# Kernel tuning notes

Hardware: AMD Instinct MI355X
Metric: run time of the kernel (lower is better)

The kernel has to match this reference:

```python
import jax, jax.numpy as jnp
import numpy as np

B, S, D = 64, 2048, 512

def setup_inputs() -> dict:
    key = jax.random.key(0)
    k1, k2 = jax.random.split(key)
    features = jax.random.normal(k1, (B, S, D), dtype=jnp.float32)
    # lengths in [1, S] so every sample has at least one valid timestep
    lengths = jax.random.randint(k2, (B,), 1, S + 1, dtype=jnp.int64)
    return {"features": features, "lengths": lengths}

def reference(features, lengths):
    # mask[b, s] = s < lengths[b]
    mask = (jnp.arange(features.shape[1])[None, :] < lengths[:, None])  # [B, S]
    masked_sum = jnp.einsum('bsd,bs->bd', features, mask.astype(features.dtype))
    pooled = masked_sum / lengths.astype(features.dtype)[:, None]  # [B, D]
    return pooled
```

## Files before the change

kernel.cpp:

```cpp
#include <hip/hip_runtime.h>


#define DDIM 512
#define TPB  128
#define NSPLIT_MAX 32

__device__ __forceinline__ void acc4(float4& a, const float4& v) {
    a.x += v.x; a.y += v.y; a.z += v.z; a.w += v.w;
}

__global__ void __launch_bounds__(TPB)
pool_partial(const float* __restrict__ feat, const int* __restrict__ lengths,
             float* __restrict__ ws, int S, int nsplit, int chunk) {
    const int b     = blockIdx.x;
    const int split = blockIdx.y;
    const int tid   = threadIdx.x;
    const int len   = lengths[b];

    const int s0 = split * chunk;
    const int s1 = min(s0 + chunk, len);

    float4 a0 = {0.f, 0.f, 0.f, 0.f};
    float4 a1 = {0.f, 0.f, 0.f, 0.f};
    float4 a2 = {0.f, 0.f, 0.f, 0.f};
    float4 a3 = {0.f, 0.f, 0.f, 0.f};

    const float4* __restrict__ base =
        reinterpret_cast<const float4*>(feat + (size_t)b * S * DDIM) + tid;
    const int ld4 = DDIM / 4;

    int s = s0;
    for (; s + 3 < s1; s += 4) {
        float4 v0 = base[(size_t)(s + 0) * ld4];
        float4 v1 = base[(size_t)(s + 1) * ld4];
        float4 v2 = base[(size_t)(s + 2) * ld4];
        float4 v3 = base[(size_t)(s + 3) * ld4];
        acc4(a0, v0); acc4(a1, v1); acc4(a2, v2); acc4(a3, v3);
    }
    for (; s < s1; ++s) {
        float4 v = base[(size_t)s * ld4];
        acc4(a0, v);
    }
    acc4(a0, a1); acc4(a2, a3); acc4(a0, a2);

    float4* wsp = reinterpret_cast<float4*>(ws + ((size_t)b * nsplit + split) * DDIM) + tid;
    *wsp = a0;
}

__global__ void __launch_bounds__(TPB)
pool_final(const float* __restrict__ ws, const int* __restrict__ lengths,
           float* __restrict__ out, int nsplit) {
    const int b   = blockIdx.x;
    const int tid = threadIdx.x;
    float4 acc = {0.f, 0.f, 0.f, 0.f};
    const float4* wsp = reinterpret_cast<const float4*>(ws + (size_t)b * nsplit * DDIM) + tid;
    for (int p = 0; p < nsplit; ++p) {
        acc4(acc, wsp[(size_t)p * (DDIM / 4)]);
    }
    const float inv = 1.0f / (float)lengths[b];
    float4 r = {acc.x * inv, acc.y * inv, acc.z * inv, acc.w * inv};
    reinterpret_cast<float4*>(out + (size_t)b * DDIM)[tid] = r;
}

__global__ void __launch_bounds__(TPB)
pool_direct(const float* __restrict__ feat, const int* __restrict__ lengths,
            float* __restrict__ out, int S) {
    const int b   = blockIdx.x;
    const int tid = threadIdx.x;
    const int len = lengths[b];
    float4 a0 = {0.f, 0.f, 0.f, 0.f};
    float4 a1 = {0.f, 0.f, 0.f, 0.f};
    float4 a2 = {0.f, 0.f, 0.f, 0.f};
    float4 a3 = {0.f, 0.f, 0.f, 0.f};
    const float4* __restrict__ base =
        reinterpret_cast<const float4*>(feat + (size_t)b * S * DDIM) + tid;
    const int ld4 = DDIM / 4;
    int s = 0;
    for (; s + 3 < len; s += 4) {
        float4 v0 = base[(size_t)(s + 0) * ld4];
        float4 v1 = base[(size_t)(s + 1) * ld4];
        float4 v2 = base[(size_t)(s + 2) * ld4];
        float4 v3 = base[(size_t)(s + 3) * ld4];
        acc4(a0, v0); acc4(a1, v1); acc4(a2, v2); acc4(a3, v3);
    }
    for (; s < len; ++s) { float4 v = base[(size_t)s * ld4]; acc4(a0, v); }
    acc4(a0, a1); acc4(a2, a3); acc4(a0, a2);
    const float inv = 1.0f / (float)len;
    float4 r = {a0.x * inv, a0.y * inv, a0.z * inv, a0.w * inv};
    reinterpret_cast<float4*>(out + (size_t)b * DDIM)[tid] = r;
}

extern "C" void kernel_launch(void* const* d_in, const int* in_sizes, int n_in,
                              void* d_out, int out_size, void* d_ws, size_t ws_size,
                              hipStream_t stream) {
    const float* feat    = (const float*)d_in[0];
    const int*   lengths = (const int*)d_in[1];
    float*       out     = (float*)d_out;

    const int B = in_sizes[1];
    const int S = in_sizes[0] / (B * DDIM);

    const size_t per_split = (size_t)B * DDIM * sizeof(float);
    int nsplit = (int)(ws_size / per_split);
    if (nsplit > NSPLIT_MAX) nsplit = NSPLIT_MAX;

    if (nsplit >= 2) {
        const int chunk = (S + nsplit - 1) / nsplit;
        float* ws = (float*)d_ws;
        dim3 grid1(B, nsplit);
        pool_partial<<<grid1, TPB, 0, stream>>>(feat, lengths, ws, S, nsplit, chunk);
        pool_final<<<B, TPB, 0, stream>>>(ws, lengths, out, nsplit);
    } else {
        pool_direct<<<B, TPB, 0, stream>>>(feat, lengths, out, S);
    }
}
```

Measured before the change: 36.12 us.

## Replace two-pass split reduction with length-balanced atomic accumulation

```diff
diff --git a/kernel.cpp b/kernel.cpp
--- a/kernel.cpp
+++ b/kernel.cpp
@@ -3,21 +3,23 @@
 
 #define DDIM 512
 #define TPB  128
-#define NSPLIT_MAX 32
+#define NSPLIT 32
 
 __device__ __forceinline__ void acc4(float4& a, const float4& v) {
     a.x += v.x; a.y += v.y; a.z += v.z; a.w += v.w;
 }
 
 __global__ void __launch_bounds__(TPB)
-pool_partial(const float* __restrict__ feat, const int* __restrict__ lengths,
-             float* __restrict__ ws, int S, int nsplit, int chunk) {
+pool_atomic(const float* __restrict__ feat, const int* __restrict__ lengths,
+            float* __restrict__ out, int S) {
     const int b     = blockIdx.x;
     const int split = blockIdx.y;
     const int tid   = threadIdx.x;
     const int len   = lengths[b];
 
+    const int chunk = (len + NSPLIT - 1) / NSPLIT;
     const int s0 = split * chunk;
+    if (s0 >= len) return;
     const int s1 = min(s0 + chunk, len);
 
     float4 a0 = {0.f, 0.f, 0.f, 0.f};
@@ -30,12 +32,17 @@
     const int ld4 = DDIM / 4;
 
     int s = s0;
-    for (; s + 3 < s1; s += 4) {
+    for (; s + 7 < s1; s += 8) {
         float4 v0 = base[(size_t)(s + 0) * ld4];
         float4 v1 = base[(size_t)(s + 1) * ld4];
         float4 v2 = base[(size_t)(s + 2) * ld4];
         float4 v3 = base[(size_t)(s + 3) * ld4];
+        float4 v4 = base[(size_t)(s + 4) * ld4];
+        float4 v5 = base[(size_t)(s + 5) * ld4];
+        float4 v6 = base[(size_t)(s + 6) * ld4];
+        float4 v7 = base[(size_t)(s + 7) * ld4];
         acc4(a0, v0); acc4(a1, v1); acc4(a2, v2); acc4(a3, v3);
+        acc4(a0, v4); acc4(a1, v5); acc4(a2, v6); acc4(a3, v7);
     }
     for (; s < s1; ++s) {
         float4 v = base[(size_t)s * ld4];
@@ -43,23 +50,12 @@
     }
     acc4(a0, a1); acc4(a2, a3); acc4(a0, a2);
 
-    float4* wsp = reinterpret_cast<float4*>(ws + ((size_t)b * nsplit + split) * DDIM) + tid;
-    *wsp = a0;
-}
-
-__global__ void __launch_bounds__(TPB)
-pool_final(const float* __restrict__ ws, const int* __restrict__ lengths,
-           float* __restrict__ out, int nsplit) {
-    const int b   = blockIdx.x;
-    const int tid = threadIdx.x;
-    float4 acc = {0.f, 0.f, 0.f, 0.f};
-    const float4* wsp = reinterpret_cast<const float4*>(ws + (size_t)b * nsplit * DDIM) + tid;
-    for (int p = 0; p < nsplit; ++p) {
-        acc4(acc, wsp[(size_t)p * (DDIM / 4)]);
-    }
-    const float inv = 1.0f / (float)lengths[b];
-    float4 r = {acc.x * inv, acc.y * inv, acc.z * inv, acc.w * inv};
-    reinterpret_cast<float4*>(out + (size_t)b * DDIM)[tid] = r;
+    const float inv = 1.0f / (float)len;
+    float* op = out + (size_t)b * DDIM + tid * 4;
+    __hip_atomic_fetch_add(op + 0, a0.x * inv, __ATOMIC_RELAXED, __HIP_MEMORY_SCOPE_AGENT);
+    __hip_atomic_fetch_add(op + 1, a0.y * inv, __ATOMIC_RELAXED, __HIP_MEMORY_SCOPE_AGENT);
+    __hip_atomic_fetch_add(op + 2, a0.z * inv, __ATOMIC_RELAXED, __HIP_MEMORY_SCOPE_AGENT);
+    __hip_atomic_fetch_add(op + 3, a0.w * inv, __ATOMIC_RELAXED, __HIP_MEMORY_SCOPE_AGENT);
 }
 
 __global__ void __launch_bounds__(TPB)
@@ -100,16 +96,10 @@
     const int B = in_sizes[1];
     const int S = in_sizes[0] / (B * DDIM);
 
-    const size_t per_split = (size_t)B * DDIM * sizeof(float);
-    int nsplit = (int)(ws_size / per_split);
-    if (nsplit > NSPLIT_MAX) nsplit = NSPLIT_MAX;
-
-    if (nsplit >= 2) {
-        const int chunk = (S + nsplit - 1) / nsplit;
-        float* ws = (float*)d_ws;
-        dim3 grid1(B, nsplit);
-        pool_partial<<<grid1, TPB, 0, stream>>>(feat, lengths, ws, S, nsplit, chunk);
-        pool_final<<<B, TPB, 0, stream>>>(ws, lengths, out, nsplit);
+    if (out_size == B * DDIM && in_sizes[0] == B * S * DDIM) {
+        hipMemsetAsync(out, 0, (size_t)out_size * sizeof(float), stream);
+        dim3 grid(B, NSPLIT);
+        pool_atomic<<<grid, TPB, 0, stream>>>(feat, lengths, out, S);
     } else {
         pool_direct<<<B, TPB, 0, stream>>>(feat, lengths, out, S);
     }
```

After: 42.87 us. 1.19x slower.

## Split sequence by per-sample length and tile D across blocks with in-block reduction

Applied to the files above, without the earlier changes.

```diff
diff --git a/kernel.cpp b/kernel.cpp
--- a/kernel.cpp
+++ b/kernel.cpp
@@ -2,8 +2,10 @@
 
 
 #define DDIM 512
+#define LD4  (DDIM / 4)
+#define NS   8
+#define DQ   4
 #define TPB  128
-#define NSPLIT_MAX 32
 
 __device__ __forceinline__ void acc4(float4& a, const float4& v) {
     a.x += v.x; a.y += v.y; a.z += v.z; a.w += v.w;
@@ -11,55 +13,88 @@
 
 __global__ void __launch_bounds__(TPB)
 pool_partial(const float* __restrict__ feat, const int* __restrict__ lengths,
-             float* __restrict__ ws, int S, int nsplit, int chunk) {
+             float* __restrict__ ws, int S) {
     const int b     = blockIdx.x;
-    const int split = blockIdx.y;
-    const int tid   = threadIdx.x;
+    const int q     = blockIdx.y;
+    const int split = blockIdx.z;
+    const int t     = threadIdx.x;
+    const int lane  = t & 31;
+    const int rg    = t >> 5;
+
     const int len   = lengths[b];
+    const int chunk = (len + NS - 1) / NS;
+    const int s0 = split * chunk;
+    if (s0 >= len) return;
+    const int s1 = min(s0 + chunk, len);
 
-    const int s0 = split * chunk;
-    const int s1 = min(s0 + chunk, len);
+    const int col = q * 32 + lane;
+    const float4* __restrict__ base =
+        reinterpret_cast<const float4*>(feat + (size_t)b * S * DDIM) + col;
 
     float4 a0 = {0.f, 0.f, 0.f, 0.f};
     float4 a1 = {0.f, 0.f, 0.f, 0.f};
     float4 a2 = {0.f, 0.f, 0.f, 0.f};
     float4 a3 = {0.f, 0.f, 0.f, 0.f};
 
-    const float4* __restrict__ base =
-        reinterpret_cast<const float4*>(feat + (size_t)b * S * DDIM) + tid;
-    const int ld4 = DDIM / 4;
-
-    int s = s0;
-    for (; s + 3 < s1; s += 4) {
-        float4 v0 = base[(size_t)(s + 0) * ld4];
-        float4 v1 = base[(size_t)(s + 1) * ld4];
-        float4 v2 = base[(size_t)(s + 2) * ld4];
-        float4 v3 = base[(size_t)(s + 3) * ld4];
+    int s = s0 + rg;
+    for (; s + 12 < s1; s += 16) {
+        float4 v0 = base[(size_t)(s +  0) * LD4];
+        float4 v1 = base[(size_t)(s +  4) * LD4];
+        float4 v2 = base[(size_t)(s +  8) * LD4];
+        float4 v3 = base[(size_t)(s + 12) * LD4];
         acc4(a0, v0); acc4(a1, v1); acc4(a2, v2); acc4(a3, v3);
     }
-    for (; s < s1; ++s) {
-        float4 v = base[(size_t)s * ld4];
+    for (; s < s1; s += 4) {
+        float4 v = base[(size_t)s * LD4];
         acc4(a0, v);
     }
     acc4(a0, a1); acc4(a2, a3); acc4(a0, a2);
 
-    float4* wsp = reinterpret_cast<float4*>(ws + ((size_t)b * nsplit + split) * DDIM) + tid;
-    *wsp = a0;
+    __shared__ float4 red[TPB];
+    red[t] = a0;
+    __syncthreads();
+    if (rg == 0) {
+        acc4(a0, red[t + 32]);
+        acc4(a0, red[t + 64]);
+        acc4(a0, red[t + 96]);
+        float4* wsp = reinterpret_cast<float4*>(ws) + ((size_t)b * NS + split) * LD4 + col;
+        *wsp = a0;
+    }
 }
 
 __global__ void __launch_bounds__(TPB)
 pool_final(const float* __restrict__ ws, const int* __restrict__ lengths,
-           float* __restrict__ out, int nsplit) {
-    const int b   = blockIdx.x;
-    const int tid = threadIdx.x;
-    float4 acc = {0.f, 0.f, 0.f, 0.f};
-    const float4* wsp = reinterpret_cast<const float4*>(ws + (size_t)b * nsplit * DDIM) + tid;
-    for (int p = 0; p < nsplit; ++p) {
-        acc4(acc, wsp[(size_t)p * (DDIM / 4)]);
+           float* __restrict__ out) {
+    const int b    = blockIdx.x;
+    const int q    = blockIdx.y;
+    const int t    = threadIdx.x;
+    const int lane = t & 31;
+    const int rg   = t >> 5;
+    const int col  = q * 32 + lane;
+
+    const int len   = lengths[b];
+    const int chunk = (len + NS - 1) / NS;
+    const int nact  = (len + chunk - 1) / chunk;
+
+    const float4* __restrict__ wsp =
+        reinterpret_cast<const float4*>(ws) + (size_t)b * NS * LD4 + col;
+
+    float4 a = {0.f, 0.f, 0.f, 0.f};
+    for (int p = rg; p < nact; p += 4) {
+        acc4(a, wsp[(size_t)p * LD4]);
     }
-    const float inv = 1.0f / (float)lengths[b];
-    float4 r = {acc.x * inv, acc.y * inv, acc.z * inv, acc.w * inv};
-    reinterpret_cast<float4*>(out + (size_t)b * DDIM)[tid] = r;
+
+    __shared__ float4 red[TPB];
+    red[t] = a;
+    __syncthreads();
+    if (rg == 0) {
+        acc4(a, red[t + 32]);
+        acc4(a, red[t + 64]);
+        acc4(a, red[t + 96]);
+        const float inv = 1.0f / (float)len;
+        float4 r = {a.x * inv, a.y * inv, a.z * inv, a.w * inv};
+        reinterpret_cast<float4*>(out + (size_t)b * DDIM)[col] = r;
+    }
 }
 
 __global__ void __launch_bounds__(TPB)
@@ -74,16 +109,15 @@
     float4 a3 = {0.f, 0.f, 0.f, 0.f};
     const float4* __restrict__ base =
         reinterpret_cast<const float4*>(feat + (size_t)b * S * DDIM) + tid;
-    const int ld4 = DDIM / 4;
     int s = 0;
     for (; s + 3 < len; s += 4) {
-        float4 v0 = base[(size_t)(s + 0) * ld4];
-        float4 v1 = base[(size_t)(s + 1) * ld4];
-        float4 v2 = base[(size_t)(s + 2) * ld4];
-        float4 v3 = base[(size_t)(s + 3) * ld4];
+        float4 v0 = base[(size_t)(s + 0) * LD4];
+        float4 v1 = base[(size_t)(s + 1) * LD4];
+        float4 v2 = base[(size_t)(s + 2) * LD4];
+        float4 v3 = base[(size_t)(s + 3) * LD4];
         acc4(a0, v0); acc4(a1, v1); acc4(a2, v2); acc4(a3, v3);
     }
-    for (; s < len; ++s) { float4 v = base[(size_t)s * ld4]; acc4(a0, v); }
+    for (; s < len; ++s) { float4 v = base[(size_t)s * LD4]; acc4(a0, v); }
     acc4(a0, a1); acc4(a2, a3); acc4(a0, a2);
     const float inv = 1.0f / (float)len;
     float4 r = {a0.x * inv, a0.y * inv, a0.z * inv, a0.w * inv};
@@ -100,16 +134,14 @@
     const int B = in_sizes[1];
     const int S = in_sizes[0] / (B * DDIM);
 
-    const size_t per_split = (size_t)B * DDIM * sizeof(float);
-    int nsplit = (int)(ws_size / per_split);
-    if (nsplit > NSPLIT_MAX) nsplit = NSPLIT_MAX;
+    const size_t need = (size_t)B * NS * DDIM * sizeof(float);
 
-    if (nsplit >= 2) {
-        const int chunk = (S + nsplit - 1) / nsplit;
+    if (ws_size >= need && out_size == B * DDIM) {
         float* ws = (float*)d_ws;
-        dim3 grid1(B, nsplit);
-        pool_partial<<<grid1, TPB, 0, stream>>>(feat, lengths, ws, S, nsplit, chunk);
-        pool_final<<<B, TPB, 0, stream>>>(ws, lengths, out, nsplit);
+        dim3 grid1(B, DQ, NS);
+        dim3 grid2(B, DQ);
+        pool_partial<<<grid1, TPB, 0, stream>>>(feat, lengths, ws, S);
+        pool_final<<<grid2, TPB, 0, stream>>>(ws, lengths, out);
     } else {
         pool_direct<<<B, TPB, 0, stream>>>(feat, lengths, out, S);
     }
```

Result: faster. 29.52 us (median of 2 runs) (-18.3%).
